# Performance work log

Measured on AMD Instinct MI355X. Metric: run time of the kernel, lower is better.

## Reference

```python
import jax, jax.numpy as jnp
import numpy as np

NUM_USER = 100000
NUM_ITEM = 50000
N = NUM_USER + NUM_ITEM
E = 1200000
D = 64          # emb_size
F_ITEM = 384    # raw item multimodal feature dim
K = 3           # number of global embedding rows (summed over dim 0)
N_LAYERS = 4
EPS = 1e-8      # F.cosine_similarity default eps


def setup_inputs() -> dict:
    key = jax.random.key(0)
    ks = jax.random.split(key, 9)
    return {
        "adj_row": jax.random.randint(ks[0], (E,), 0, N),
        "adj_col": jax.random.randint(ks[1], (E,), 0, N),
        # scaled like a degree-normalized adjacency (avg degree ~8)
        "adj_val": jax.random.uniform(ks[2], (E,), jnp.float32) / 8.0,
        "user_fea": jax.random.normal(ks[3], (NUM_USER, D), jnp.float32) * 0.1,
        "item_fea": jax.random.normal(ks[4], (NUM_ITEM, F_ITEM), jnp.float32) * 0.1,
        "g_emb_u": jax.random.normal(ks[5], (K, D), jnp.float32) * 0.1,
        "g_emb_i": jax.random.normal(ks[6], (K, D), jnp.float32) * 0.1,
        "mlp_w": jax.random.normal(ks[7], (D, F_ITEM), jnp.float32) * (1.0 / np.sqrt(F_ITEM)),
        "mlp_b": jnp.zeros((D,), jnp.float32),
    }


def _cosine_sim(a, b):
    # matches F.cosine_similarity(a, b, dim=-1) with eps clamp on norms
    na = jnp.maximum(jnp.linalg.norm(a, axis=-1), EPS)
    nb = jnp.maximum(jnp.linalg.norm(b, axis=-1), EPS)
    return jnp.sum(a * b, axis=-1) / (na * nb)


def reference(adj_row, adj_col, adj_val, user_fea, item_fea, g_emb_u, g_emb_i, mlp_w, mlp_b):
    # global embeddings summed over modality dim
    user_emb = user_fea + jnp.sum(g_emb_u, axis=0)                       # [U, D]
    item_emb = jnp.tanh(item_fea @ mlp_w.T + mlp_b) + jnp.sum(g_emb_i, axis=0)  # [I, D]
    ego = jnp.concatenate([user_emb, item_emb], axis=0)                  # [N, D]

    x = ego
    acc = ego  # sum over layers, includes layer-0 (ego) term
    for _ in range(N_LAYERS):
        # sparse adj @ x as gather -> scale -> segment-sum scatter
        x = jax.ops.segment_sum(adj_val[:, None] * x[adj_col], adj_row, num_segments=N)
        w = _cosine_sim(x, ego)     # [N]
        x = w[:, None] * x          # einsum('a,ab->ab')
        acc = acc + x

    return acc[:NUM_USER], acc[NUM_USER:]
```

## Files before the change

### kernel.cpp

```cpp
#include <hip/hip_runtime.h>
#include <hip/hip_bf16.h>

#define U_NUM 100000
#define I_NUM 50000
#define N_NUM 150000
#define E_NUM 1200000
#define D 64
#define F_IT 384
#define CAP 32
#define EPSV 1e-8f
#define FXS 524288.0f
#define FXI (1.0f / 524288.0f)

#define NBIN 586
#define RPB 256
#define FBLK 586
#define CELL_CAP 8
#define OV_CAP 256

typedef unsigned short ushort_t;
typedef unsigned int uint_t;
typedef short bf16x8 __attribute__((ext_vector_type(8)));
typedef float f32x4 __attribute__((ext_vector_type(4)));

__device__ __forceinline__ ushort_t f2bf(float f) {
    uint_t x = __float_as_uint(f);
    uint_t r = x + 0x7fffu + ((x >> 16) & 1u);
    return (ushort_t)(r >> 16);
}
__device__ __forceinline__ float bfu2f(uint_t u_lo16) {
    return __uint_as_float(u_lo16 << 16);
}
__device__ __forceinline__ void dec4(uint2 u, float* f) {
    f[0] = bfu2f(u.x & 0xffffu); f[1] = bfu2f(u.x >> 16);
    f[2] = bfu2f(u.y & 0xffffu); f[3] = bfu2f(u.y >> 16);
}

__global__ void k_prep(const float* __restrict__ w, const float* __restrict__ gu,
                       const float* __restrict__ gi,
                       short* __restrict__ wbf, float* __restrict__ gsu,
                       float* __restrict__ gsi, int* __restrict__ ovcnt) {
    int b = blockIdx.x, t = threadIdx.x;
    if (b < 96) {
        int i = b * 256 + t;
        wbf[i] = (short)f2bf(w[i]);
    } else {
        if (t < 64) gsu[t] = gu[t] + gu[64 + t] + gu[128 + t];
        else if (t < 128) { int d = t - 64; gsi[d] = gi[d] + gi[64 + d] + gi[128 + d]; }
        for (int i = t; i < NBIN; i += 256) ovcnt[i] = 0;
    }
}

__global__ __launch_bounds__(256) void k_fill(
        const int* __restrict__ row, const int* __restrict__ col,
        const float* __restrict__ val,
        int2* __restrict__ cellbuf, int* __restrict__ cellcnt,
        int* __restrict__ ovcnt, int2* __restrict__ ovbuf) {
    __shared__ int bincnt[NBIN];
    int fid = blockIdx.x, tid = threadIdx.x;
    for (int i = tid; i < NBIN; i += 256) bincnt[i] = 0;
    __syncthreads();
    int t = fid * 256 + tid;
    if (t < E_NUM / 8) {
        int r[8], c[8];
        float v[8];
#pragma unroll
        for (int k = 0; k < 8; k++) {
            int e = k * (E_NUM / 8) + t;
            r[k] = row[e]; c[k] = col[e]; v[k] = val[e];
        }
#pragma unroll
        for (int k = 0; k < 8; k++) {
            int bn = r[k] >> 8;
            int key = c[k] | ((r[k] & 255) << 18);
            int ls = atomicAdd(&bincnt[bn], 1);
            if (ls < CELL_CAP) {
                cellbuf[((size_t)fid * NBIN + bn) * CELL_CAP + ls] =
                    make_int2(key, __float_as_int(v[k]));
            } else {
                int o = atomicAdd(&ovcnt[bn], 1);
                if (o < OV_CAP) ovbuf[bn * OV_CAP + o] = make_int2(key, __float_as_int(v[k]));
            }
        }
    }
    __syncthreads();
    for (int i = tid; i < NBIN; i += 256)
        cellcnt[(size_t)fid * NBIN + i] = min(bincnt[i], CELL_CAP);
}

#define ITEM_B 782
__global__ __launch_bounds__(256) void k_item(
        const float* __restrict__ ifea, const float* __restrict__ bvec,
        const short* __restrict__ wbf, const float* __restrict__ gsi,
        float* __restrict__ ego, ushort_t* __restrict__ egob) {
    int iid = blockIdx.x;
    int tid = threadIdx.x;
    int wave = tid >> 6, lane = tid & 63;
    int q = lane >> 4, m = lane & 15;
    int ibase = iid * 64 + wave * 16;
    int irow = min(ibase + m, I_NUM - 1);
    const float* arow = ifea + (size_t)irow * F_IT + q * 8;

    f32x4 av[4];
#pragma unroll
    for (int n = 0; n < 4; n++) av[n] = (f32x4){0.f, 0.f, 0.f, 0.f};
    float4 nfa0 = ((const float4*)(arow))[0];
    float4 nfa1 = ((const float4*)(arow))[1];
#pragma unroll
    for (int c = 0; c < 12; c++) {
        float4 fa0 = nfa0, fa1 = nfa1;
        if (c < 11) {
            nfa0 = ((const float4*)(arow + (c + 1) * 32))[0];
            nfa1 = ((const float4*)(arow + (c + 1) * 32))[1];
        }
        bf16x8 af;
        af[0] = (short)f2bf(fa0.x); af[1] = (short)f2bf(fa0.y);
        af[2] = (short)f2bf(fa0.z); af[3] = (short)f2bf(fa0.w);
        af[4] = (short)f2bf(fa1.x); af[5] = (short)f2bf(fa1.y);
        af[6] = (short)f2bf(fa1.z); af[7] = (short)f2bf(fa1.w);
#pragma unroll
        for (int n = 0; n < 4; n++) {
            bf16x8 bf = *(const bf16x8*)(wbf + (size_t)(n * 16 + m) * F_IT + c * 32 + q * 8);
            av[n] = __builtin_amdgcn_mfma_f32_16x16x32_bf16(af, bf, av[n], 0, 0, 0);
        }
    }
#pragma unroll
    for (int n = 0; n < 4; n++) {
        int dim = n * 16 + m;
        float bb = bvec[dim];
        float gg = gsi[dim];
#pragma unroll
        for (int rr = 0; rr < 4; rr++) {
            int item = ibase + q * 4 + rr;
            if (item < I_NUM) {
                float v = tanhf(av[n][rr] + bb) + gg;
                size_t o = (size_t)(U_NUM + item) * D + dim;
                ego[o] = v;
                egob[o] = f2bf(v);
            }
        }
    }
}

#define USER_B 1563
__global__ __launch_bounds__(256) void k_user(
        const float* __restrict__ ufea, const float* __restrict__ gsu,
        float* __restrict__ ego, ushort_t* __restrict__ egob) {
    int t = blockIdx.x * 256 + threadIdx.x;
    size_t base = (size_t)t * 16;
    if (base >= (size_t)U_NUM * D) return;
    int d0 = (int)(base & 63);
    float f[16];
#pragma unroll
    for (int k = 0; k < 4; k++) {
        float4 v = ((const float4*)(ufea + base))[k];
        f[4 * k] = v.x; f[4 * k + 1] = v.y; f[4 * k + 2] = v.z; f[4 * k + 3] = v.w;
    }
#pragma unroll
    for (int j = 0; j < 16; j++) f[j] += gsu[d0 + j];
#pragma unroll
    for (int k = 0; k < 4; k++) {
        ((float4*)(ego + base))[k] = make_float4(f[4 * k], f[4 * k + 1], f[4 * k + 2], f[4 * k + 3]);
    }
    uint4 u0, u1;
    u0.x = (uint_t)f2bf(f[0]) | ((uint_t)f2bf(f[1]) << 16);
    u0.y = (uint_t)f2bf(f[2]) | ((uint_t)f2bf(f[3]) << 16);
    u0.z = (uint_t)f2bf(f[4]) | ((uint_t)f2bf(f[5]) << 16);
    u0.w = (uint_t)f2bf(f[6]) | ((uint_t)f2bf(f[7]) << 16);
    u1.x = (uint_t)f2bf(f[8]) | ((uint_t)f2bf(f[9]) << 16);
    u1.y = (uint_t)f2bf(f[10]) | ((uint_t)f2bf(f[11]) << 16);
    u1.z = (uint_t)f2bf(f[12]) | ((uint_t)f2bf(f[13]) << 16);
    u1.w = (uint_t)f2bf(f[14]) | ((uint_t)f2bf(f[15]) << 16);
    ((uint4*)(egob + base))[0] = u0;
    ((uint4*)(egob + base))[1] = u1;
}

__global__ __launch_bounds__(256) void k_bucket(const int2* __restrict__ cellbuf,
                                                const int* __restrict__ cellcnt,
                                                const int* __restrict__ ovcnt,
                                                const int2* __restrict__ ovbuf,
                                                int* __restrict__ cnt,
                                                int2* __restrict__ bkt) {
    __shared__ int lc[RPB];
    int bn = blockIdx.x, tid = threadIdx.x;
    lc[tid] = 0;
    __syncthreads();
    int rbase = bn << 8;
#pragma unroll
    for (int h = 0; h < 3; h++) {
        int f = h * 256 + tid;
        if (f < FBLK) {
            int c = cellcnt[(size_t)f * NBIN + bn];
            const int2* cp = cellbuf + ((size_t)f * NBIN + bn) * CELL_CAP;
            for (int i = 0; i < c; i++) {
                int2 e = cp[i];
                int rl = e.x >> 18;
                int s = atomicAdd(&lc[rl], 1);
                if (s < CAP) bkt[(size_t)(rbase + rl) * CAP + s] = make_int2(e.x & 0x3ffff, e.y);
            }
        }
    }
    int oc = min(ovcnt[bn], OV_CAP);
    for (int i = tid; i < oc; i += 256) {
        int2 e = ovbuf[bn * OV_CAP + i];
        int rl = e.x >> 18;
        int s = atomicAdd(&lc[rl], 1);
        if (s < CAP) bkt[(size_t)(rbase + rl) * CAP + s] = make_int2(e.x & 0x3ffff, e.y);
    }
    __syncthreads();
    int r = rbase + tid;
    if (r < N_NUM) {
        int d = min(lc[tid], CAP);
        int dp = (d <= 16) ? 16 : 32;
        for (int s = d; s < dp; s++)
            bkt[(size_t)r * CAP + s] = make_int2(0, 0);
        cnt[r] = dp;
    }
}

#define ACC4(A, VS, X) \
    A[0] += __float2int_rn(VS * bfu2f(X.x & 0xffffu)); A[1] += __float2int_rn(VS * bfu2f(X.x >> 16)); \
    A[2] += __float2int_rn(VS * bfu2f(X.y & 0xffffu)); A[3] += __float2int_rn(VS * bfu2f(X.y >> 16));

__device__ __forceinline__ float row_weight16(const float* a, const float* e) {
    float dot = 0.f, nx = 0.f, ne = 0.f;
#pragma unroll
    for (int j = 0; j < 4; j++) {
        dot += a[j] * e[j]; nx += a[j] * a[j]; ne += e[j] * e[j];
    }
#pragma unroll
    for (int m = 1; m < 16; m <<= 1) {
        dot += __shfl_xor(dot, m);
        nx  += __shfl_xor(nx, m);
        ne  += __shfl_xor(ne, m);
    }
    return dot / (fmaxf(sqrtf(nx), EPSV) * fmaxf(sqrtf(ne), EPSV));
}

__device__ __forceinline__ void gather16(const ushort_t* __restrict__ xb,
                                         const int4* __restrict__ cp, int l,
                                         int* __restrict__ a) {
    int4 p[8];
#pragma unroll
    for (int j = 0; j < 8; j++) p[j] = cp[j];
    uint2 xu[16];
#pragma unroll
    for (int j = 0; j < 8; j++) {
        xu[2 * j]     = ((const uint2*)xb)[(size_t)p[j].x * 16 + l];
        xu[2 * j + 1] = ((const uint2*)xb)[(size_t)p[j].z * 16 + l];
    }
#pragma unroll
    for (int j = 0; j < 8; j++) {
        float va = __int_as_float(p[j].y) * FXS;
        float vb = __int_as_float(p[j].w) * FXS;
        ACC4(a, va, xu[2 * j]);
        ACC4(a, vb, xu[2 * j + 1]);
    }
}

__device__ __forceinline__ void spmm_body(const ushort_t* __restrict__ xb,
                                          const ushort_t* __restrict__ egob,
                                          const int* __restrict__ cnt,
                                          const int2* __restrict__ bkt,
                                          ushort_t* __restrict__ xob) {
    int t = blockIdx.x * 256 + threadIdx.x;
    int l = t & 15, r = t >> 4;
    if (r >= N_NUM) return;
    int dp = cnt[r];
    const int4* cp = (const int4*)(bkt + (size_t)r * CAP);
    int a[4] = {0, 0, 0, 0};
    gather16(xb, cp, l, a);
    if (dp > 16) gather16(xb, cp + 8, l, a);
    float af[4];
#pragma unroll
    for (int j = 0; j < 4; j++) af[j] = (float)a[j] * FXI;
    float e[4]; dec4(((const uint2*)egob)[(size_t)r * 16 + l], e);
    float wgt = row_weight16(af, e);
    uint2 ov;
    ov.x = (uint_t)f2bf(wgt * af[0]) | ((uint_t)f2bf(wgt * af[1]) << 16);
    ov.y = (uint_t)f2bf(wgt * af[2]) | ((uint_t)f2bf(wgt * af[3]) << 16);
    ((uint2*)xob)[(size_t)r * 16 + l] = ov;
}

__global__ __launch_bounds__(256) void k_spmmA(const ushort_t* __restrict__ xb,
        const ushort_t* __restrict__ egob, const int* __restrict__ cnt,
        const int2* __restrict__ bkt, ushort_t* __restrict__ xob)
{ spmm_body(xb, egob, cnt, bkt, xob); }

__global__ __launch_bounds__(256) void k_spmmB(const ushort_t* __restrict__ xb,
        const ushort_t* __restrict__ egob, const int* __restrict__ cnt,
        const int2* __restrict__ bkt, ushort_t* __restrict__ xob)
{ spmm_body(xb, egob, cnt, bkt, xob); }

__global__ __launch_bounds__(256) void k_spmmC(const ushort_t* __restrict__ xb,
        const ushort_t* __restrict__ egob, const int* __restrict__ cnt,
        const int2* __restrict__ bkt, ushort_t* __restrict__ xob)
{ spmm_body(xb, egob, cnt, bkt, xob); }

__global__ __launch_bounds__(256) void k_spmm4(const ushort_t* __restrict__ x3,
                                               const ushort_t* __restrict__ x1,
                                               const ushort_t* __restrict__ x2,
                                               const float* __restrict__ ego,
                                               const int* __restrict__ cnt,
                                               const int2* __restrict__ bkt,
                                               float* __restrict__ out) {
    int t = blockIdx.x * 256 + threadIdx.x;
    int l = t & 15, r = t >> 4;
    if (r >= N_NUM) return;
    int dp = cnt[r];
    const int4* cp = (const int4*)(bkt + (size_t)r * CAP);
    int a[4] = {0, 0, 0, 0};
    gather16(x3, cp, l, a);
    if (dp > 16) gather16(x3, cp + 8, l, a);
    float af[4];
#pragma unroll
    for (int j = 0; j < 4; j++) af[j] = (float)a[j] * FXI;
    float4 ev = ((const float4*)ego)[(size_t)r * 16 + l];
    float e[4] = {ev.x, ev.y, ev.z, ev.w};
    float wgt = row_weight16(af, e);
    float x1d[4], x2d[4], x3d[4];
    dec4(((const uint2*)x1)[(size_t)r * 16 + l], x1d);
    dec4(((const uint2*)x2)[(size_t)r * 16 + l], x2d);
    dec4(((const uint2*)x3)[(size_t)r * 16 + l], x3d);
    float s[4];
#pragma unroll
    for (int j = 0; j < 4; j++) s[j] = e[j] + x1d[j] + x2d[j] + x3d[j] + wgt * af[j];
    ((float4*)out)[(size_t)r * 16 + l] = make_float4(s[0], s[1], s[2], s[3]);
}

extern "C" void kernel_launch(void* const* d_in, const int* in_sizes, int n_in,
                              void* d_out, int out_size, void* d_ws, size_t ws_size,
                              hipStream_t stream) {
    const int*   adj_row  = (const int*)d_in[0];
    const int*   adj_col  = (const int*)d_in[1];
    const float* adj_val  = (const float*)d_in[2];
    const float* user_fea = (const float*)d_in[3];
    const float* item_fea = (const float*)d_in[4];
    const float* gu       = (const float*)d_in[5];
    const float* gi       = (const float*)d_in[6];
    const float* mlp_w    = (const float*)d_in[7];
    const float* mlp_b    = (const float*)d_in[8];

    float* out = (float*)d_out;

    char* ws = (char*)d_ws;
    size_t off = 0;
    float*    ego  = (float*)(ws + off);    off += (size_t)N_NUM * D * 4;
    ushort_t* egob = (ushort_t*)(ws + off); off += (size_t)N_NUM * D * 2;
    size_t x1off = off;
    ushort_t* x1   = (ushort_t*)(ws + off); off += (size_t)N_NUM * D * 2;
    ushort_t* x2   = (ushort_t*)(ws + off); off += (size_t)N_NUM * D * 2;
    ushort_t* x3   = (ushort_t*)(ws + off); off += (size_t)N_NUM * D * 2;
    int*      cnt  = (int*)(ws + off);      off += (size_t)N_NUM * 4;
    short*    wbf  = (short*)(ws + off);    off += (size_t)D * F_IT * 2;
    float*    gsu  = (float*)(ws + off);    off += 64 * 4;
    float*    gsi  = (float*)(ws + off);    off += 64 * 4;
    off = (off + 255) & ~(size_t)255;
    int2*     bkt  = (int2*)(ws + off);     off += (size_t)N_NUM * CAP * 8;
    int*      cellcnt = (int*)(ws + off);   off += (size_t)FBLK * NBIN * 4;
    int*      ovcnt   = (int*)(ws + off);   off += (size_t)NBIN * 4;
    int2*     ovbuf   = (int2*)(ws + off);  off += (size_t)NBIN * OV_CAP * 8;
    int2*     cellbuf = (int2*)(ws + x1off);

    k_prep<<<97, 256, 0, stream>>>(mlp_w, gu, gi, wbf, gsu, gsi, ovcnt);
    k_fill<<<FBLK, 256, 0, stream>>>(adj_row, adj_col, adj_val,
                                     cellbuf, cellcnt, ovcnt, ovbuf);
    k_item<<<ITEM_B, 256, 0, stream>>>(item_fea, mlp_b, wbf, gsi, ego, egob);
    k_user<<<USER_B, 256, 0, stream>>>(user_fea, gsu, ego, egob);
    k_bucket<<<NBIN, 256, 0, stream>>>(cellbuf, cellcnt, ovcnt, ovbuf, cnt, bkt);
    int g16 = ((size_t)N_NUM * 16 + 255) / 256;
    k_spmmA<<<g16, 256, 0, stream>>>(egob, egob, cnt, bkt, x1);
    k_spmmB<<<g16, 256, 0, stream>>>(x1,   egob, cnt, bkt, x2);
    k_spmmC<<<g16, 256, 0, stream>>>(x2,   egob, cnt, bkt, x3);
    k_spmm4<<<g16, 256, 0, stream>>>(x3, x1, x2, ego, cnt, bkt, out);
}
```

Baseline: 394.3 us.

## Merge independent prep kernels into two interleaved horizontally fused launches

Combines the edge-fill and user-embedding kernels into one launch, and the item MLP and bucket kernels into another, with block slots interleaved by group so the different workloads share the GPU at once. This removes two kernel launches and the idle tail between small dependent kernels, letting the memory-bound and compute-bound pieces overlap. The cost is mixed block types with different register and shared-memory needs, which may lower occupancy for the fused kernels.

```diff
diff --git a/kernel.cpp b/kernel.cpp
--- a/kernel.cpp
+++ b/kernel.cpp
@@ -17,6 +17,11 @@
 #define FBLK 586
 #define CELL_CAP 8
 #define OV_CAP 256
+
+#define ITEM_B 782
+#define USER_B 1563
+#define FU_GRP 196
+#define BI_GRP 196
 
 typedef unsigned short ushort_t;
 typedef unsigned int uint_t;
@@ -51,170 +56,178 @@
     }
 }
 
-__global__ __launch_bounds__(256) void k_fill(
+__global__ __launch_bounds__(256) void k_fu(
         const int* __restrict__ row, const int* __restrict__ col,
         const float* __restrict__ val,
+        const float* __restrict__ ufea, const float* __restrict__ gsu,
         int2* __restrict__ cellbuf, int* __restrict__ cellcnt,
-        int* __restrict__ ovcnt, int2* __restrict__ ovbuf) {
+        int* __restrict__ ovcnt, int2* __restrict__ ovbuf,
+        float* __restrict__ ego, ushort_t* __restrict__ egob) {
     __shared__ int bincnt[NBIN];
-    int fid = blockIdx.x, tid = threadIdx.x;
-    for (int i = tid; i < NBIN; i += 256) bincnt[i] = 0;
-    __syncthreads();
-    int t = fid * 256 + tid;
-    if (t < E_NUM / 8) {
-        int r[8], c[8];
-        float v[8];
-#pragma unroll
-        for (int k = 0; k < 8; k++) {
-            int e = k * (E_NUM / 8) + t;
-            r[k] = row[e]; c[k] = col[e]; v[k] = val[e];
-        }
-#pragma unroll
-        for (int k = 0; k < 8; k++) {
-            int bn = r[k] >> 8;
-            int key = c[k] | ((r[k] & 255) << 18);
-            int ls = atomicAdd(&bincnt[bn], 1);
-            if (ls < CELL_CAP) {
-                cellbuf[((size_t)fid * NBIN + bn) * CELL_CAP + ls] =
-                    make_int2(key, __float_as_int(v[k]));
-            } else {
-                int o = atomicAdd(&ovcnt[bn], 1);
-                if (o < OV_CAP) ovbuf[bn * OV_CAP + o] = make_int2(key, __float_as_int(v[k]));
-            }
-        }
-    }
-    __syncthreads();
-    for (int i = tid; i < NBIN; i += 256)
-        cellcnt[(size_t)fid * NBIN + i] = min(bincnt[i], CELL_CAP);
-}
-
-#define ITEM_B 782
-__global__ __launch_bounds__(256) void k_item(
+    int b = blockIdx.x;
+    int grp = b / 11, slot = b % 11;
+    int tid = threadIdx.x;
+
+    if (slot < 3) {
+        int fid = grp * 3 + slot;
+        if (fid >= FBLK) return;
+        for (int i = tid; i < NBIN; i += 256) bincnt[i] = 0;
+        __syncthreads();
+        int t = fid * 256 + tid;
+        if (t < E_NUM / 8) {
+            int r[8], c[8];
+            float v[8];
+#pragma unroll
+            for (int k = 0; k < 8; k++) {
+                int e = k * (E_NUM / 8) + t;
+                r[k] = row[e]; c[k] = col[e]; v[k] = val[e];
+            }
+#pragma unroll
+            for (int k = 0; k < 8; k++) {
+                int bn = r[k] >> 8;
+                int key = c[k] | ((r[k] & 255) << 18);
+                int ls = atomicAdd(&bincnt[bn], 1);
+                if (ls < CELL_CAP) {
+                    cellbuf[((size_t)fid * NBIN + bn) * CELL_CAP + ls] =
+                        make_int2(key, __float_as_int(v[k]));
+                } else {
+                    int o = atomicAdd(&ovcnt[bn], 1);
+                    if (o < OV_CAP) ovbuf[bn * OV_CAP + o] = make_int2(key, __float_as_int(v[k]));
+                }
+            }
+        }
+        __syncthreads();
+        for (int i = tid; i < NBIN; i += 256)
+            cellcnt[(size_t)fid * NBIN + i] = min(bincnt[i], CELL_CAP);
+    } else {
+        int uid = grp * 8 + (slot - 3);
+        if (uid >= USER_B) return;
+        int t = uid * 256 + tid;
+        size_t base = (size_t)t * 16;
+        if (base >= (size_t)U_NUM * D) return;
+        int d0 = (int)(base & 63);
+        float f[16];
+#pragma unroll
+        for (int k = 0; k < 4; k++) {
+            float4 v = ((const float4*)(ufea + base))[k];
+            f[4 * k] = v.x; f[4 * k + 1] = v.y; f[4 * k + 2] = v.z; f[4 * k + 3] = v.w;
+        }
+#pragma unroll
+        for (int j = 0; j < 16; j++) f[j] += gsu[d0 + j];
+#pragma unroll
+        for (int k = 0; k < 4; k++) {
+            ((float4*)(ego + base))[k] = make_float4(f[4 * k], f[4 * k + 1], f[4 * k + 2], f[4 * k + 3]);
+        }
+        uint4 u0, u1;
+        u0.x = (uint_t)f2bf(f[0]) | ((uint_t)f2bf(f[1]) << 16);
+        u0.y = (uint_t)f2bf(f[2]) | ((uint_t)f2bf(f[3]) << 16);
+        u0.z = (uint_t)f2bf(f[4]) | ((uint_t)f2bf(f[5]) << 16);
+        u0.w = (uint_t)f2bf(f[6]) | ((uint_t)f2bf(f[7]) << 16);
+        u1.x = (uint_t)f2bf(f[8]) | ((uint_t)f2bf(f[9]) << 16);
+        u1.y = (uint_t)f2bf(f[10]) | ((uint_t)f2bf(f[11]) << 16);
+        u1.z = (uint_t)f2bf(f[12]) | ((uint_t)f2bf(f[13]) << 16);
+        u1.w = (uint_t)f2bf(f[14]) | ((uint_t)f2bf(f[15]) << 16);
+        ((uint4*)(egob + base))[0] = u0;
+        ((uint4*)(egob + base))[1] = u1;
+    }
+}
+
+__global__ __launch_bounds__(256) void k_bi(
         const float* __restrict__ ifea, const float* __restrict__ bvec,
         const short* __restrict__ wbf, const float* __restrict__ gsi,
+        const int2* __restrict__ cellbuf, const int* __restrict__ cellcnt,
+        const int* __restrict__ ovcnt, const int2* __restrict__ ovbuf,
+        int* __restrict__ cnt, int2* __restrict__ bkt,
         float* __restrict__ ego, ushort_t* __restrict__ egob) {
-    int iid = blockIdx.x;
+    __shared__ int lc[RPB];
+    int b = blockIdx.x;
+    int grp = b / 7, slot = b % 7;
     int tid = threadIdx.x;
-    int wave = tid >> 6, lane = tid & 63;
-    int q = lane >> 4, m = lane & 15;
-    int ibase = iid * 64 + wave * 16;
-    int irow = min(ibase + m, I_NUM - 1);
-    const float* arow = ifea + (size_t)irow * F_IT + q * 8;
-
-    f32x4 av[4];
-#pragma unroll
-    for (int n = 0; n < 4; n++) av[n] = (f32x4){0.f, 0.f, 0.f, 0.f};
-    float4 nfa0 = ((const float4*)(arow))[0];
-    float4 nfa1 = ((const float4*)(arow))[1];
-#pragma unroll
-    for (int c = 0; c < 12; c++) {
-        float4 fa0 = nfa0, fa1 = nfa1;
-        if (c < 11) {
-            nfa0 = ((const float4*)(arow + (c + 1) * 32))[0];
-            nfa1 = ((const float4*)(arow + (c + 1) * 32))[1];
-        }
-        bf16x8 af;
-        af[0] = (short)f2bf(fa0.x); af[1] = (short)f2bf(fa0.y);
-        af[2] = (short)f2bf(fa0.z); af[3] = (short)f2bf(fa0.w);
-        af[4] = (short)f2bf(fa1.x); af[5] = (short)f2bf(fa1.y);
-        af[6] = (short)f2bf(fa1.z); af[7] = (short)f2bf(fa1.w);
+
+    if (slot < 4) {
+        int iid = grp * 4 + slot;
+        if (iid >= ITEM_B) return;
+        int wave = tid >> 6, lane = tid & 63;
+        int q = lane >> 4, m = lane & 15;
+        int ibase = iid * 64 + wave * 16;
+        int irow = min(ibase + m, I_NUM - 1);
+        const float* arow = ifea + (size_t)irow * F_IT + q * 8;
+
+        f32x4 av[4];
+#pragma unroll
+        for (int n = 0; n < 4; n++) av[n] = (f32x4){0.f, 0.f, 0.f, 0.f};
+        float4 nfa0 = ((const float4*)(arow))[0];
+        float4 nfa1 = ((const float4*)(arow))[1];
+#pragma unroll
+        for (int c = 0; c < 12; c++) {
+            float4 fa0 = nfa0, fa1 = nfa1;
+            if (c < 11) {
+                nfa0 = ((const float4*)(arow + (c + 1) * 32))[0];
+                nfa1 = ((const float4*)(arow + (c + 1) * 32))[1];
+            }
+            bf16x8 af;
+            af[0] = (short)f2bf(fa0.x); af[1] = (short)f2bf(fa0.y);
+            af[2] = (short)f2bf(fa0.z); af[3] = (short)f2bf(fa0.w);
+            af[4] = (short)f2bf(fa1.x); af[5] = (short)f2bf(fa1.y);
+            af[6] = (short)f2bf(fa1.z); af[7] = (short)f2bf(fa1.w);
+#pragma unroll
+            for (int n = 0; n < 4; n++) {
+                bf16x8 bf = *(const bf16x8*)(wbf + (size_t)(n * 16 + m) * F_IT + c * 32 + q * 8);
+                av[n] = __builtin_amdgcn_mfma_f32_16x16x32_bf16(af, bf, av[n], 0, 0, 0);
+            }
+        }
 #pragma unroll
         for (int n = 0; n < 4; n++) {
-            bf16x8 bf = *(const bf16x8*)(wbf + (size_t)(n * 16 + m) * F_IT + c * 32 + q * 8);
-            av[n] = __builtin_amdgcn_mfma_f32_16x16x32_bf16(af, bf, av[n], 0, 0, 0);
-        }
-    }
-#pragma unroll
-    for (int n = 0; n < 4; n++) {
-        int dim = n * 16 + m;
-        float bb = bvec[dim];
-        float gg = gsi[dim];
-#pragma unroll
-        for (int rr = 0; rr < 4; rr++) {
-            int item = ibase + q * 4 + rr;
-            if (item < I_NUM) {
-                float v = tanhf(av[n][rr] + bb) + gg;
-                size_t o = (size_t)(U_NUM + item) * D + dim;
-                ego[o] = v;
-                egob[o] = f2bf(v);
-            }
-        }
-    }
-}
-
-#define USER_B 1563
-__global__ __launch_bounds__(256) void k_user(
-        const float* __restrict__ ufea, const float* __restrict__ gsu,
-        float* __restrict__ ego, ushort_t* __restrict__ egob) {
-    int t = blockIdx.x * 256 + threadIdx.x;
-    size_t base = (size_t)t * 16;
-    if (base >= (size_t)U_NUM * D) return;
-    int d0 = (int)(base & 63);
-    float f[16];
-#pragma unroll
-    for (int k = 0; k < 4; k++) {
-        float4 v = ((const float4*)(ufea + base))[k];
-        f[4 * k] = v.x; f[4 * k + 1] = v.y; f[4 * k + 2] = v.z; f[4 * k + 3] = v.w;
-    }
-#pragma unroll
-    for (int j = 0; j < 16; j++) f[j] += gsu[d0 + j];
-#pragma unroll
-    for (int k = 0; k < 4; k++) {
-        ((float4*)(ego + base))[k] = make_float4(f[4 * k], f[4 * k + 1], f[4 * k + 2], f[4 * k + 3]);
-    }
-    uint4 u0, u1;
-    u0.x = (uint_t)f2bf(f[0]) | ((uint_t)f2bf(f[1]) << 16);
-    u0.y = (uint_t)f2bf(f[2]) | ((uint_t)f2bf(f[3]) << 16);
-    u0.z = (uint_t)f2bf(f[4]) | ((uint_t)f2bf(f[5]) << 16);
-    u0.w = (uint_t)f2bf(f[6]) | ((uint_t)f2bf(f[7]) << 16);
-    u1.x = (uint_t)f2bf(f[8]) | ((uint_t)f2bf(f[9]) << 16);
-    u1.y = (uint_t)f2bf(f[10]) | ((uint_t)f2bf(f[11]) << 16);
-    u1.z = (uint_t)f2bf(f[12]) | ((uint_t)f2bf(f[13]) << 16);
-    u1.w = (uint_t)f2bf(f[14]) | ((uint_t)f2bf(f[15]) << 16);
-    ((uint4*)(egob + base))[0] = u0;
-    ((uint4*)(egob + base))[1] = u1;
-}
-
-__global__ __launch_bounds__(256) void k_bucket(const int2* __restrict__ cellbuf,
-                                                const int* __restrict__ cellcnt,
-                                                const int* __restrict__ ovcnt,
-                                                const int2* __restrict__ ovbuf,
-                                                int* __restrict__ cnt,
-                                                int2* __restrict__ bkt) {
-    __shared__ int lc[RPB];
-    int bn = blockIdx.x, tid = threadIdx.x;
-    lc[tid] = 0;
-    __syncthreads();
-    int rbase = bn << 8;
-#pragma unroll
-    for (int h = 0; h < 3; h++) {
-        int f = h * 256 + tid;
-        if (f < FBLK) {
-            int c = cellcnt[(size_t)f * NBIN + bn];
-            const int2* cp = cellbuf + ((size_t)f * NBIN + bn) * CELL_CAP;
-            for (int i = 0; i < c; i++) {
-                int2 e = cp[i];
-                int rl = e.x >> 18;
-                int s = atomicAdd(&lc[rl], 1);
-                if (s < CAP) bkt[(size_t)(rbase + rl) * CAP + s] = make_int2(e.x & 0x3ffff, e.y);
-            }
-        }
-    }
-    int oc = min(ovcnt[bn], OV_CAP);
-    for (int i = tid; i < oc; i += 256) {
-        int2 e = ovbuf[bn * OV_CAP + i];
-        int rl = e.x >> 18;
-        int s = atomicAdd(&lc[rl], 1);
-        if (s < CAP) bkt[(size_t)(rbase + rl) * CAP + s] = make_int2(e.x & 0x3ffff, e.y);
-    }
-    __syncthreads();
-    int r = rbase + tid;
-    if (r < N_NUM) {
-        int d = min(lc[tid], CAP);
-        int dp = (d <= 16) ? 16 : 32;
-        for (int s = d; s < dp; s++)
-            bkt[(size_t)r * CAP + s] = make_int2(0, 0);
-        cnt[r] = dp;
+            int dim = n * 16 + m;
+            float bb = bvec[dim];
+            float gg = gsi[dim];
+#pragma unroll
+            for (int rr = 0; rr < 4; rr++) {
+                int item = ibase + q * 4 + rr;
+                if (item < I_NUM) {
+                    float v = tanhf(av[n][rr] + bb) + gg;
+                    size_t o = (size_t)(U_NUM + item) * D + dim;
+                    ego[o] = v;
+                    egob[o] = f2bf(v);
+                }
+            }
+        }
+    } else {
+        int bn = grp * 3 + (slot - 4);
+        if (bn >= NBIN) return;
+        lc[tid] = 0;
+        __syncthreads();
+        int rbase = bn << 8;
+#pragma unroll
+        for (int h = 0; h < 3; h++) {
+            int f = h * 256 + tid;
+            if (f < FBLK) {
+                int c = cellcnt[(size_t)f * NBIN + bn];
+                const int2* cp = cellbuf + ((size_t)f * NBIN + bn) * CELL_CAP;
+                for (int i = 0; i < c; i++) {
+                    int2 e = cp[i];
+                    int rl = e.x >> 18;
+                    int s = atomicAdd(&lc[rl], 1);
+                    if (s < CAP) bkt[(size_t)(rbase + rl) * CAP + s] = make_int2(e.x & 0x3ffff, e.y);
+                }
+            }
+        }
+        int oc = min(ovcnt[bn], OV_CAP);
+        for (int i = tid; i < oc; i += 256) {
+            int2 e = ovbuf[bn * OV_CAP + i];
+            int rl = e.x >> 18;
+            int s = atomicAdd(&lc[rl], 1);
+            if (s < CAP) bkt[(size_t)(rbase + rl) * CAP + s] = make_int2(e.x & 0x3ffff, e.y);
+        }
+        __syncthreads();
+        int r = rbase + tid;
+        if (r < N_NUM) {
+            int d = min(lc[tid], CAP);
+            int dp = (d <= 16) ? 16 : 32;
+            for (int s = d; s < dp; s++)
+                bkt[(size_t)r * CAP + s] = make_int2(0, 0);
+            cnt[r] = dp;
+        }
     }
 }
 
@@ -363,11 +376,12 @@
     int2*     cellbuf = (int2*)(ws + x1off);
 
     k_prep<<<97, 256, 0, stream>>>(mlp_w, gu, gi, wbf, gsu, gsi, ovcnt);
-    k_fill<<<FBLK, 256, 0, stream>>>(adj_row, adj_col, adj_val,
-                                     cellbuf, cellcnt, ovcnt, ovbuf);
-    k_item<<<ITEM_B, 256, 0, stream>>>(item_fea, mlp_b, wbf, gsi, ego, egob);
-    k_user<<<USER_B, 256, 0, stream>>>(user_fea, gsu, ego, egob);
-    k_bucket<<<NBIN, 256, 0, stream>>>(cellbuf, cellcnt, ovcnt, ovbuf, cnt, bkt);
+    k_fu<<<FU_GRP * 11, 256, 0, stream>>>(adj_row, adj_col, adj_val,
+                                          user_fea, gsu,
+                                          cellbuf, cellcnt, ovcnt, ovbuf, ego, egob);
+    k_bi<<<BI_GRP * 7, 256, 0, stream>>>(item_fea, mlp_b, wbf, gsi,
+                                         cellbuf, cellcnt, ovcnt, ovbuf,
+                                         cnt, bkt, ego, egob);
     int g16 = ((size_t)N_NUM * 16 + 255) / 256;
     k_spmmA<<<g16, 256, 0, stream>>>(egob, egob, cnt, bkt, x1);
     k_spmmB<<<g16, 256, 0, stream>>>(x1,   egob, cnt, bkt, x2);
```

After: 398.7 us. Within noise of the previous version (+1.1%).
